# Optimization experiments

Measured on AMD Instinct MI355X. Metric: run time of the kernel, lower is better.

The kernel has to match this reference:

```python
import jax, jax.numpy as jnp
import numpy as np

B, C, L = 32, 64, 4096
LEVEL, FL, DIM, HID = 3, 8, 64, 64
MID = max(1, C // 4)
REG = 0.01
ODE_STEPS, ODE_H = 10, 0.1  # fixed-step integration of t in [0,1] (eval_t final point)


def _gelu(x):
    return jax.nn.gelu(x, approximate=False)  # torch nn.GELU default is exact erf


def _conv1d(x, w, b, pad, mode):
    # x: [B,Cin,L], w: [Cout,Cin,K] -> [B,Cout,L] (cross-correlation, like torch)
    if pad:
        x = jnp.pad(x, ((0, 0), (0, 0), (pad, pad)), mode=mode)
    y = jax.lax.conv_general_dilated(x, w, (1,), 'VALID',
                                     dimension_numbers=('NCH', 'OIH', 'NCH'))
    return y + b[None, :, None]


def _conv1x1(x, w, b):
    return jnp.einsum('oc,bcl->bol', w, x) + b[None, :, None]


def setup_inputs() -> dict:
    key = jax.random.key(0)
    ks = jax.random.split(key, 12)
    rn = lambda k, s: jax.random.normal(k, s, jnp.float32) * 0.05
    return {
        'x': jax.random.normal(ks[0], (B, C, L), jnp.float32),
        'ode_c1_w': rn(ks[1], (DIM, C, 3)),
        'ode_c1_b': jnp.zeros((DIM,), jnp.float32),
        'ode_c2_w': rn(ks[2], (C, DIM, 3)),
        'ode_c2_b': jnp.zeros((C,), jnp.float32),
        'damp': jnp.float32(0.01),
        'stat_w': rn(ks[3], (HID, C)),
        'stat_b': jnp.zeros((HID,), jnp.float32),
        'gen1_w': rn(ks[4], (2 * HID, HID)),
        'gen1_b': jnp.zeros((2 * HID,), jnp.float32),
        'gen2_w': rn(ks[5], (2 * FL, 2 * HID)),
        'gen2_b': jnp.zeros((2 * FL,), jnp.float32),
        'gate_w': rn(ks[6], (LEVEL, C, C, 3)),
        'gate_b': jnp.zeros((LEVEL, C), jnp.float32),
        'att_w1': rn(ks[7], (LEVEL - 1, MID, C)),
        'att_b1': jnp.zeros((LEVEL - 1, MID), jnp.float32),
        'att_w2': rn(ks[8], (LEVEL - 1, C, MID)),
        'att_b2': jnp.zeros((LEVEL - 1, C), jnp.float32),
    }


def _forward(x, ode_c1_w, ode_c1_b, ode_c2_w, ode_c2_b, damp,
             stat_w, stat_b, gen1_w, gen1_b, gen2_w, gen2_b,
             gate_w, gate_b, att_w1, att_b1, att_w2, att_b2):
    # --- WaveletODE_Pro: autonomous vector field, fixed-step RK4 over [0,1] ---
    def f(z):
        h = _gelu(_conv1d(z, ode_c1_w, ode_c1_b, 1, 'edge'))
        h = jnp.tanh(_conv1d(h, ode_c2_w, ode_c2_b, 1, 'edge'))
        return h - damp * z

    def rk4(z, _):
        k1 = f(z)
        k2 = f(z + 0.5 * ODE_H * k1)
        k3 = f(z + 0.5 * ODE_H * k2)
        k4 = f(z + ODE_H * k3)
        return z + (ODE_H / 6.0) * (k1 + 2 * k2 + 2 * k3 + k4), None

    x_evolved, _ = jax.lax.scan(rk4, x, None, length=ODE_STEPS)

    # --- DyWAN_Pro: per-sample wavelet filter generation + regularizers ---
    def dywan(a):
        stat = _gelu(a.mean(-1) @ stat_w.T + stat_b)               # [B,HID]
        g = _gelu(stat @ gen1_w.T + gen1_b) @ gen2_w.T + gen2_b     # [B,2F]
        lo, hi = g[:, :FL], g[:, FL:]
        lo_pad = jnp.pad(lo, ((0, 0), (1, 1)))                      # zero pad=1, kernel [-1,1]
        lo_smooth = jnp.abs(lo_pad[:, 1:] - lo_pad[:, :-1]).mean()
        lo_n = lo / (jnp.linalg.norm(lo, axis=1, keepdims=True) + 1e-8)
        shift = sum(jnp.abs(lo_n[:, :, None] * jnp.roll(lo_n, s, axis=1)[:, None, :]).mean()
                    for s in range(1, 4))
        amp = jnp.abs((lo_n ** 2).sum(1) - 1.0).mean()
        return lo, hi, REG * (shift + amp) + 0.1 * lo_smooth

    pad_l, pad_r = FL // 2, FL - FL // 2 - 1
    approx = x_evolved
    details, los, his = [], [], []
    ortho = jnp.float32(0.0)
    for _ in range(LEVEL):
        lo, hi, o = dywan(approx)
        ortho = ortho + o
        los.append(lo)
        his.append(hi)
        ap = jnp.pad(approx, ((0, 0), (0, 0), (pad_l, pad_r)), mode='edge')
        # per-sample filter shared across channels: grouped conv == windowed einsum
        win = jnp.stack([ap[:, :, k:k + L] for k in range(FL)], axis=-1)  # [B,C,L,F]
        new_approx = jnp.einsum('bclk,bk->bcl', win, lo)
        details.append(jnp.einsum('bclk,bk->bcl', win, hi))
        approx = new_approx

    # --- CrossScaleFusion: yl input is the INITIAL evolved approx (coeffs[0]) ---
    cur = x_evolved
    enhanced = []
    for i in range(LEVEL - 1, -1, -1):
        det = details[i]
        if i < LEVEL - 1:
            att = jax.nn.sigmoid(_conv1x1(_gelu(_conv1x1(cur, att_w1[i], att_b1[i])),
                                          att_w2[i], att_b2[i]))
            det = det * att + det
        gate = jax.nn.sigmoid(_conv1d(cur, gate_w[i], gate_b[i], 1, 'constant'))
        cur = cur + gate * det
        enhanced.append(det)
    enhanced.reverse()
    return (cur, enhanced[0], enhanced[1], enhanced[2], ortho,
            jnp.stack(los), jnp.stack(his))


def reference(x, ode_c1_w, ode_c1_b, ode_c2_w, ode_c2_b, damp,
              stat_w, stat_b, gen1_w, gen1_b, gen2_w, gen2_b,
              gate_w, gate_b, att_w1, att_b1, att_w2, att_b2):
    return _forward(x, ode_c1_w, ode_c1_b, ode_c2_w, ode_c2_b, damp,
                    stat_w, stat_b, gen1_w, gen1_b, gen2_w, gen2_b,
                    gate_w, gate_b, att_w1, att_b1, att_w2, att_b2)
```

## Files before the change

### kernel.cpp

```cpp
#include <hip/hip_runtime.h>

#define Bn   32
#define Cn   64
#define Ln   4096
#define Nn   (Bn*Cn*Ln)
#define FLn  8
#define MIDn 16
#define TILE3 64
#define NT   64

typedef __bf16 bf16_t;
typedef bf16_t bf16x4 __attribute__((ext_vector_type(4)));
typedef bf16_t bf16x8 __attribute__((ext_vector_type(8)));
typedef float  f32x4  __attribute__((ext_vector_type(4)));

__device__ __forceinline__ float tanh_fast(float x) {
    float t = __expf(2.0f * x);
    return 1.0f - __fdividef(2.0f, 1.0f + t);
}
__device__ __forceinline__ float gelu_fast(float x) {
    return __fdividef(x, 1.0f + __expf(-1.702f * x));
}
__device__ __forceinline__ float sigmoid_f(float x) {
    return 1.0f / (1.0f + __expf(-x));
}

__global__ __launch_bounds__(256) void prep_weights(
    const float* __restrict__ w1, const float* __restrict__ w2,
    const float* __restrict__ gw, const float* __restrict__ aw1,
    const float* __restrict__ aw2,
    bf16_t* __restrict__ w1f, bf16_t* __restrict__ w2f,
    bf16_t* __restrict__ gwf, bf16_t* __restrict__ aw1f,
    float* __restrict__ aw2t)
{
    int idx = blockIdx.x*256 + threadIdx.x;
    if (idx < 1536) {
        int lane = idx & 63;
        int f  = (idx >> 6) % 6;
        int mt = (idx >> 6) / 6;
        int tau = f >> 1, kc = f & 1;
        int oc = mt*16 + (lane & 15);
        int c0 = kc*32 + (lane >> 4)*8;
        #pragma unroll
        for (int e = 0; e < 8; ++e) {
            int c = c0 + e;
            w1f[idx*8 + e] = (bf16_t)w1[oc*192 + c*3 + tau];
            w2f[idx*8 + e] = (bf16_t)w2[oc*192 + c*3 + tau];
        }
    }
    if (idx < 4608) {
        int lane = idx & 63;
        int r  = idx >> 6;
        int f  = r % 6;
        int mt = (r / 6) % 4;
        int lvl = r / 24;
        int tau = f >> 1, kc = f & 1;
        int oc = mt*16 + (lane & 15);
        int c0 = kc*32 + (lane >> 4)*8;
        #pragma unroll
        for (int e = 0; e < 8; ++e)
            gwf[idx*8 + e] = (bf16_t)gw[((lvl*64 + oc)*64 + (c0+e))*3 + tau];
    }
    if (idx < 256) {
        int lane = idx & 63;
        int kc  = (idx >> 6) & 1;
        int lvl = idx >> 7;
        int mm = lane & 15;
        int c0 = kc*32 + (lane >> 4)*8;
        #pragma unroll
        for (int e = 0; e < 8; ++e)
            aw1f[idx*8 + e] = (bf16_t)aw1[lvl*1024 + mm*64 + c0 + e];
    }
    if (idx < 2*64*16) {
        int lvl = idx / 1024, rem = idx % 1024;
        int oc = rem / 16, mm = rem % 16;
        aw2t[lvl*1024 + mm*64 + oc] = aw2[idx];
    }
}

__global__ __launch_bounds__(256, 2) void ode_rk4_step(
    const float* __restrict__ zsrc, float* __restrict__ zdst,
    const bf16_t* __restrict__ w1f, const float* __restrict__ b1,
    const bf16_t* __restrict__ w2f, const float* __restrict__ b2,
    const float* __restrict__ damp_p)
{
    __shared__ bf16_t ZC[80*64];
    __shared__ bf16_t HT[80*64];
    __shared__ bf16_t Z0[80*64];
    __shared__ bf16_t SUMB[64*64];

    const int tid  = threadIdx.x;
    const int w    = tid >> 6;
    const int lane = tid & 63;
    const int c15  = lane & 15;
    const int hb   = lane >> 4;
    const int oc0  = w*16 + hb*4;
    const int b    = blockIdx.y;
    const int l0   = blockIdx.x * NT;
    const size_t bbase = (size_t)b * Cn * Ln;
    const float damp = damp_p[0];
    const int pmin = (blockIdx.x == 0) ? 8 : 0;
    const int pmax = (blockIdx.x == gridDim.x - 1) ? 71 : 79;

    #pragma unroll
    for (int jj = 0; jj < 4; ++jj) {
        const int cc0 = (w << 4) + jj*4;
        const float* zr0 = zsrc + bbase + (size_t)(cc0+0) * Ln;
        const float* zr1 = zsrc + bbase + (size_t)(cc0+1) * Ln;
        const float* zr2 = zsrc + bbase + (size_t)(cc0+2) * Ln;
        const float* zr3 = zsrc + bbase + (size_t)(cc0+3) * Ln;
        #pragma unroll
        for (int m2 = 0; m2 < 2; ++m2) {
            int p = lane + (m2 << 6);
            if (p < 80) {
                int l = l0 - 8 + p;
                l = l < 0 ? 0 : (l > Ln-1 ? Ln-1 : l);
                bf16x4 v;
                v[0] = (bf16_t)zr0[l]; v[1] = (bf16_t)zr1[l];
                v[2] = (bf16_t)zr2[l]; v[3] = (bf16_t)zr3[l];
                int off = p*64 + (cc0 ^ ((p & 7) << 3));
                *(bf16x4*)&ZC[off] = v;
                *(bf16x4*)&Z0[off] = v;
            }
        }
    }

    f32x4 bias1v, bias2v;
    #pragma unroll
    for (int j = 0; j < 4; ++j) {
        bias1v[j] = b1[oc0 + j];
        bias2v[j] = b2[oc0 + j];
    }
    bf16x8 af1[6], af2[6];
    {
        const bf16x8* wp1 = (const bf16x8*)w1f + (w*6)*64 + lane;
        const bf16x8* wp2 = (const bf16x8*)w2f + (w*6)*64 + lane;
        #pragma unroll
        for (int f = 0; f < 6; ++f) { af1[f] = wp1[f*64]; af2[f] = wp2[f*64]; }
    }

    __syncthreads();

    for (int i = 0; i < 4; ++i) {
        const int hLo = 2*i + 1, hHi = 79 - 2*i;
        const int kLo = 2*i + 2, kHi = 78 - 2*i;

        #pragma unroll
        for (int nt = 0; nt < 5; ++nt) {
            int ph = nt*16 + c15;
            f32x4 acc = bias1v;
            #pragma unroll
            for (int tau = 0; tau < 3; ++tau) {
                int p = ph + tau - 1;
                p = p < pmin ? pmin : (p > pmax ? pmax : p);
                int base = p*64 + ((hb*8) ^ ((p & 7) << 3));
                acc = __builtin_amdgcn_mfma_f32_16x16x32_bf16(
                    af1[tau*2+0], *(const bf16x8*)&ZC[base], acc, 0, 0, 0);
                acc = __builtin_amdgcn_mfma_f32_16x16x32_bf16(
                    af1[tau*2+1], *(const bf16x8*)&ZC[base ^ 32], acc, 0, 0, 0);
            }
            if (ph >= hLo && ph < hHi) {
                bf16x4 hv;
                #pragma unroll
                for (int j = 0; j < 4; ++j)
                    hv[j] = (bf16_t)gelu_fast(acc[j]);
                *(bf16x4*)&HT[ph*64 + (oc0 ^ ((ph & 7) << 3))] = hv;
            }
        }
        __syncthreads();

        #pragma unroll
        for (int nt = 0; nt < 5; ++nt) {
            int pk = nt*16 + c15;
            f32x4 acc = bias2v;
            #pragma unroll
            for (int tau = 0; tau < 3; ++tau) {
                int q = pk + tau - 1;
                q = q < pmin ? pmin : (q > pmax ? pmax : q);
                int base = q*64 + ((hb*8) ^ ((q & 7) << 3));
                acc = __builtin_amdgcn_mfma_f32_16x16x32_bf16(
                    af2[tau*2+0], *(const bf16x8*)&HT[base], acc, 0, 0, 0);
                acc = __builtin_amdgcn_mfma_f32_16x16x32_bf16(
                    af2[tau*2+1], *(const bf16x8*)&HT[base ^ 32], acc, 0, 0, 0);
            }
            const int col = oc0 ^ ((pk & 7) << 3);
            const int off = pk*64 + col;
            if (i < 3) {
                if (pk >= kLo && pk < kHi) {
                    bf16x4 zc = *(const bf16x4*)&ZC[off];
                    bf16x4 z0 = *(const bf16x4*)&Z0[off];
                    const float alpha = (i == 2) ? 0.10f : 0.05f;
                    const bool inS = (pk >= 8) && (pk < 72);
                    const int soff = (pk-8)*64 + col;
                    bf16x4 sv;
                    if (i > 0 && inS) sv = *(const bf16x4*)&SUMB[soff];
                    bf16x4 wv, nsv;
                    #pragma unroll
                    for (int j = 0; j < 4; ++j) {
                        float kv = tanh_fast(acc[j]) - damp * (float)zc[j];
                        wv[j]  = (bf16_t)((float)z0[j] + alpha * kv);
                        nsv[j] = (i == 0) ? (bf16_t)kv
                                          : (bf16_t)((float)sv[j] + 2.0f * kv);
                    }
                    *(bf16x4*)&ZC[off] = wv;
                    if (inS) *(bf16x4*)&SUMB[soff] = nsv;
                }
            } else {
                if (pk >= 8 && pk < 72) {
                    bf16x4 zc = *(const bf16x4*)&ZC[off];
                    bf16x4 sv = *(const bf16x4*)&SUMB[(pk-8)*64 + col];
                    int gcol = l0 + pk - 8;
                    #pragma unroll
                    for (int j = 0; j < 4; ++j) {
                        float kv = tanh_fast(acc[j]) - damp * (float)zc[j];
                        size_t gof = bbase + (size_t)(oc0 + j)*Ln + gcol;
                        zdst[gof] = zsrc[gof] + (0.1f/6.0f) * ((float)sv[j] + kv);
                    }
                }
            }
        }
        if (i < 3) __syncthreads();
    }
}

__global__ __launch_bounds__(256) void mean_kernel(const float* __restrict__ in, float* __restrict__ m)
{
    const int bc = blockIdx.x;
    const float* __restrict__ row = in + (size_t)bc*Ln;
    float s = 0.0f;
    for (int l = threadIdx.x; l < Ln; l += 256) s += row[l];
    #pragma unroll
    for (int off = 32; off > 0; off >>= 1) s += __shfl_down(s, off, 64);
    __shared__ float red[4];
    if ((threadIdx.x & 63) == 0) red[threadIdx.x >> 6] = s;
    __syncthreads();
    if (threadIdx.x == 0) m[bc] = red[0]+red[1]+red[2]+red[3];
}

__global__ __launch_bounds__(256) void dywan_kernel(
    const float* __restrict__ m,
    const float* __restrict__ stat_w, const float* __restrict__ stat_b,
    const float* __restrict__ gen1_w, const float* __restrict__ gen1_b,
    const float* __restrict__ gen2_w, const float* __restrict__ gen2_b,
    float* __restrict__ tail, int lvl)
{
    __shared__ float m_s[Bn][Cn];
    __shared__ float stat_s[Bn][64];
    __shared__ float g1_s[Bn][128];
    __shared__ float g_s[Bn][16];
    __shared__ float ored[Bn];
    const int tid = threadIdx.x;
    for (int i = tid; i < Bn*Cn; i += 256) m_s[i>>6][i&63] = m[i] * (1.0f/Ln);
    __syncthreads();
    for (int i = tid; i < Bn*64; i += 256) {
        int b = i >> 6, h = i & 63;
        float a = stat_b[h];
        for (int c = 0; c < Cn; ++c) a = fmaf(stat_w[h*64+c], m_s[b][c], a);
        stat_s[b][h] = 0.5f * a * (1.0f + erff(a * 0.7071067811865476f));
    }
    __syncthreads();
    for (int i = tid; i < Bn*128; i += 256) {
        int b = i >> 7, j = i & 127;
        float a = gen1_b[j];
        for (int h = 0; h < 64; ++h) a = fmaf(gen1_w[j*64+h], stat_s[b][h], a);
        g1_s[b][j] = 0.5f * a * (1.0f + erff(a * 0.7071067811865476f));
    }
    __syncthreads();
    for (int i = tid; i < Bn*16; i += 256) {
        int b = i >> 4, q = i & 15;
        float a = gen2_b[q];
        for (int j = 0; j < 128; ++j) a = fmaf(gen2_w[q*128+j], g1_s[b][j], a);
        g_s[b][q] = a;
    }
    __syncthreads();
    for (int i = tid; i < Bn*16; i += 256) {
        int b = i >> 4, q = i & 15;
        if (q < FLn) tail[1 + lvl*(Bn*FLn) + b*FLn + q] = g_s[b][q];
        else         tail[1 + 3*(Bn*FLn) + lvl*(Bn*FLn) + b*FLn + (q-FLn)] = g_s[b][q];
    }
    if (tid < Bn) {
        const int b = tid;
        float S1 = 0.f, n2 = 0.f, sm = 0.f, prev = 0.f;
        #pragma unroll
        for (int k = 0; k < FLn; ++k) {
            float v = g_s[b][k];
            S1 += fabsf(v); n2 = fmaf(v, v, n2);
            sm += fabsf(v - prev); prev = v;
        }
        sm += fabsf(prev);
        float den = sqrtf(n2) + 1e-8f;
        float Sn = S1 / den;
        float s2n = n2 / (den*den);
        ored[b] = 0.01f * (3.0f*Sn*Sn*(1.0f/2048.0f) + fabsf(s2n - 1.0f)*(1.0f/32.0f))
                + 0.1f * sm * (1.0f/288.0f);
    }
    __syncthreads();
    if (tid == 0) {
        float o = 0.f;
        for (int b = 0; b < Bn; ++b) o += ored[b];
        if (lvl == 0) tail[0] = o; else tail[0] += o;
    }
}

__global__ __launch_bounds__(256) void filter_kernel(
    const float* __restrict__ in, float* __restrict__ napprox,
    float* __restrict__ det,
    const float* __restrict__ lo, const float* __restrict__ hi,
    float* __restrict__ msum)
{
    const int bc = blockIdx.y;
    const int b = bc >> 6;
    float lov[8], hiv[8];
    #pragma unroll
    for (int k = 0; k < 8; ++k) { lov[k] = lo[b*8+k]; hiv[k] = hi[b*8+k]; }
    const float* __restrict__ row = in + (size_t)bc*Ln;
    const int l = blockIdx.x*256 + threadIdx.x;
    float na = 0.0f, dv = 0.0f;
    #pragma unroll
    for (int k = 0; k < 8; ++k) {
        int j = l + k - 4;
        j = j < 0 ? 0 : (j >= Ln ? Ln-1 : j);
        float v = row[j];
        na = fmaf(v, lov[k], na);
        dv = fmaf(v, hiv[k], dv);
    }
    size_t g = (size_t)bc*Ln + l;
    if (napprox) napprox[g] = na;
    det[g] = dv;
    if (msum) {
        float s = na;
        #pragma unroll
        for (int off = 32; off > 0; off >>= 1) s += __shfl_down(s, off, 64);
        __shared__ float red[4];
        if ((threadIdx.x & 63) == 0) red[threadIdx.x >> 6] = s;
        __syncthreads();
        if (threadIdx.x == 0)
            atomicAdd(&msum[bc], red[0]+red[1]+red[2]+red[3]);
    }
}

template<bool HAS_ATT>
__global__ __launch_bounds__(256, 2) void stage3_kernel(
    const float* __restrict__ cur_in, float* __restrict__ det,
    float* __restrict__ cur_out,
    const bf16_t* __restrict__ gwf, const float* __restrict__ gb,
    const bf16_t* __restrict__ aw1f, const float* __restrict__ ab1,
    const float* __restrict__ aw2t, const float* __restrict__ ab2)
{
    __shared__ bf16_t CB[66*64];
    __shared__ float t1_s[16][65];
    __shared__ float gate_s[64][65];
    __shared__ float att_s[64][65];

    const int tid  = threadIdx.x;
    const int w    = tid >> 6;
    const int lane = tid & 63;
    const int c15  = lane & 15;
    const int hb   = lane >> 4;
    const int oc0  = w*16 + hb*4;
    const int b    = blockIdx.y;
    const int l0   = blockIdx.x * TILE3;
    const size_t bbase = (size_t)b * Cn * Ln;

    #pragma unroll
    for (int jj = 0; jj < 4; ++jj) {
        const int cc0 = (w << 4) + jj*4;
        const float* cr0 = cur_in + bbase + (size_t)(cc0+0) * Ln;
        const float* cr1 = cur_in + bbase + (size_t)(cc0+1) * Ln;
        const float* cr2 = cur_in + bbase + (size_t)(cc0+2) * Ln;
        const float* cr3 = cur_in + bbase + (size_t)(cc0+3) * Ln;
        #pragma unroll
        for (int m2 = 0; m2 < 2; ++m2) {
            int p = lane + (m2 << 6);
            if (p < 66) {
                int l = l0 - 1 + p;
                bool in = (l >= 0) && (l < Ln);
                bf16x4 v;
                v[0] = (bf16_t)(in ? cr0[l] : 0.0f);
                v[1] = (bf16_t)(in ? cr1[l] : 0.0f);
                v[2] = (bf16_t)(in ? cr2[l] : 0.0f);
                v[3] = (bf16_t)(in ? cr3[l] : 0.0f);
                *(bf16x4*)&CB[p*64 + (cc0 ^ ((p & 7) << 3))] = v;
            }
        }
    }
    __syncthreads();

    if (HAS_ATT) {
        f32x4 acc;
        #pragma unroll
        for (int j = 0; j < 4; ++j) acc[j] = ab1[hb*4 + j];
        const int p = w*16 + c15 + 1;
        #pragma unroll
        for (int kc = 0; kc < 2; ++kc) {
            bf16x8 a1 = ((const bf16x8*)aw1f)[kc*64 + lane];
            int base = p*64 + (((kc*32) + hb*8) ^ ((p & 7) << 3));
            acc = __builtin_amdgcn_mfma_f32_16x16x32_bf16(
                a1, *(const bf16x8*)&CB[base], acc, 0, 0, 0);
        }
        #pragma unroll
        for (int j = 0; j < 4; ++j)
            t1_s[hb*4 + j][w*16 + c15] = gelu_fast(acc[j]);
    }

    {
        bf16x8 ag[6];
        const bf16x8* wp = (const bf16x8*)gwf + (w*6)*64 + lane;
        #pragma unroll
        for (int f = 0; f < 6; ++f) ag[f] = wp[f*64];
        f32x4 biasg;
        #pragma unroll
        for (int j = 0; j < 4; ++j) biasg[j] = gb[oc0 + j];

        #pragma unroll
        for (int nt = 0; nt < 5; ++nt) {
            int ph = nt*16 + c15;
            f32x4 acc = biasg;
            #pragma unroll
            for (int tau = 0; tau < 3; ++tau) {
                int q = ph - 1 + tau;
                q = q < 0 ? 0 : (q > 65 ? 65 : q);
                int base0 = q*64 + ((hb*8) ^ ((q & 7) << 3));
                acc = __builtin_amdgcn_mfma_f32_16x16x32_bf16(
                    ag[tau*2+0], *(const bf16x8*)&CB[base0], acc, 0, 0, 0);
                acc = __builtin_amdgcn_mfma_f32_16x16x32_bf16(
                    ag[tau*2+1], *(const bf16x8*)&CB[base0 ^ 32], acc, 0, 0, 0);
            }
            if (ph >= 1 && ph < 65) {
                int t = ph - 1;
                #pragma unroll
                for (int j = 0; j < 4; ++j)
                    gate_s[oc0 + j][t] = sigmoid_f(acc[j]);
            }
        }
    }
    __syncthreads();

    if (HAS_ATT) {
        const int oc = tid & 63;
        const int t0 = (tid >> 6) * 16;
        float w2r[16];
        #pragma unroll
        for (int mm = 0; mm < MIDn; ++mm) w2r[mm] = aw2t[mm*64 + oc];
        float av[16];
        const float bb = ab2[oc];
        #pragma unroll
        for (int j = 0; j < 16; ++j) av[j] = bb;
        #pragma unroll
        for (int mm = 0; mm < MIDn; ++mm) {
            #pragma unroll
            for (int j = 0; j < 16; ++j) av[j] = fmaf(w2r[mm], t1_s[mm][t0+j], av[j]);
        }
        #pragma unroll
        for (int j = 0; j < 16; ++j) att_s[oc][t0+j] = sigmoid_f(av[j]);
        __syncthreads();
    }

    const size_t gb0 = bbase + l0;
    for (int e = tid; e < Cn*TILE3; e += 256) {
        int c = e >> 6, t = e & 63;
        size_t g = gb0 + (size_t)c*Ln + t;
        float d = det[g];
        if (HAS_ATT) { d = d * (1.0f + att_s[c][t]); det[g] = d; }
        cur_out[g] = cur_in[g] + gate_s[c][t]*d;
    }
}

extern "C" void kernel_launch(void* const* d_in, const int* in_sizes, int n_in,
                              void* d_out, int out_size, void* d_ws, size_t ws_size,
                              hipStream_t stream)
{
    const float* x      = (const float*)d_in[0];
    const float* c1w    = (const float*)d_in[1];
    const float* c1b    = (const float*)d_in[2];
    const float* c2w    = (const float*)d_in[3];
    const float* c2b    = (const float*)d_in[4];
    const float* damp   = (const float*)d_in[5];
    const float* stat_w = (const float*)d_in[6];
    const float* stat_b = (const float*)d_in[7];
    const float* gen1_w = (const float*)d_in[8];
    const float* gen1_b = (const float*)d_in[9];
    const float* gen2_w = (const float*)d_in[10];
    const float* gen2_b = (const float*)d_in[11];
    const float* gate_w = (const float*)d_in[12];
    const float* gate_b = (const float*)d_in[13];
    const float* att_w1 = (const float*)d_in[14];
    const float* att_b1 = (const float*)d_in[15];
    const float* att_w2 = (const float*)d_in[16];
    const float* att_b2 = (const float*)d_in[17];

    float* out = (float*)d_out;
    float* Z    = (float*)d_ws;
    float* WSB  = Z + Nn;
    float* aw2t = WSB + Nn;
    float* m0   = aw2t + 2048;
    float* m1   = m0 + 2048;
    float* m2   = m1 + 2048;
    bf16_t* w1f  = (bf16_t*)(m2 + 2048);
    bf16_t* w2f  = w1f + 12288;
    bf16_t* gwf  = w2f + 12288;
    bf16_t* aw1f = gwf + 36864;

    float* tail = out + (size_t)4*Nn;

    prep_weights<<<144, 256, 0, stream>>>(c1w, c2w, gate_w, att_w1, att_w2,
                                          w1f, w2f, gwf, aw1f, aw2t);
    hipMemsetAsync(m1, 0, 2*2048*sizeof(float), stream);

    dim3 gOde(Ln/NT, Bn);
    for (int s = 0; s < 10; ++s) {
        const float* src = (s == 0) ? x : ((s & 1) ? Z : WSB);
        float*       dst = (s & 1) ? WSB : Z;
        ode_rk4_step<<<gOde, 256, 0, stream>>>(src, dst, w1f, c1b, w2f, c2b, damp);
    }

    dim3 gFil(Ln/256, Bn*Cn);
    const float* appr_in[3]  = {WSB, Z, out};
    float*       appr_out[3] = {Z, out, nullptr};
    float*       msum[3]     = {m1, m2, nullptr};
    float*       muse[3]     = {m0, m1, m2};
    mean_kernel<<<Bn*Cn, 256, 0, stream>>>(WSB, m0);
    for (int lvl = 0; lvl < 3; ++lvl) {
        dywan_kernel<<<1, 256, 0, stream>>>(muse[lvl], stat_w, stat_b, gen1_w, gen1_b,
                                            gen2_w, gen2_b, tail, lvl);
        filter_kernel<<<gFil, 256, 0, stream>>>(appr_in[lvl], appr_out[lvl],
            out + (size_t)(1+lvl)*Nn,
            tail + 1 + lvl*(Bn*FLn),
            tail + 1 + 3*(Bn*FLn) + lvl*(Bn*FLn),
            msum[lvl]);
    }

    dim3 gS3(Ln/TILE3, Bn);
    stage3_kernel<false><<<gS3, 256, 0, stream>>>(WSB, out + (size_t)3*Nn, Z,
        gwf + 2*12288, gate_b + 2*64, nullptr, nullptr, nullptr, nullptr);
    stage3_kernel<true><<<gS3, 256, 0, stream>>>(Z, out + (size_t)2*Nn, WSB,
        gwf + 1*12288, gate_b + 1*64, aw1f + 1024, att_b1 + 16, aw2t + 1024, att_b2 + 64);
    stage3_kernel<true><<<gS3, 256, 0, stream>>>(WSB, out + (size_t)1*Nn, out,
        gwf, gate_b, aw1f, att_b1, aw2t, att_b2);
}
```

Before: 1.186 ms.

## Fuse two RK4 steps per ODE kernel launch using wider halo tiles

The ODE kernel now performs two RK4 steps per launch, widening the shared-memory halo from 8 to 16 columns (96-wide tiles) so the intermediate state stays on chip. This halves the number of launches and the global round trips of the state tensor, and keeps the step-start state in fp32 in shared memory. In exchange, each block recomputes extra halo columns (6 instead of 5 column tiles per stage) and uses more LDS, which may lower occupancy.

```diff
diff --git a/kernel.cpp b/kernel.cpp
--- a/kernel.cpp
+++ b/kernel.cpp
@@ -7,7 +7,7 @@
 #define FLn  8
 #define MIDn 16
 #define TILE3 64
-#define NT   64
+#define NTD  64
 
 typedef __bf16 bf16_t;
 typedef bf16_t bf16x4 __attribute__((ext_vector_type(4)));
@@ -78,16 +78,16 @@
     }
 }
 
-__global__ __launch_bounds__(256, 2) void ode_rk4_step(
+__global__ __launch_bounds__(256, 2) void ode_rk4_2step(
     const float* __restrict__ zsrc, float* __restrict__ zdst,
     const bf16_t* __restrict__ w1f, const float* __restrict__ b1,
     const bf16_t* __restrict__ w2f, const float* __restrict__ b2,
     const float* __restrict__ damp_p)
 {
-    __shared__ bf16_t ZC[80*64];
-    __shared__ bf16_t HT[80*64];
-    __shared__ bf16_t Z0[80*64];
-    __shared__ bf16_t SUMB[64*64];
+    __shared__ bf16_t ZC[96*64];
+    __shared__ bf16_t HT[96*64];
+    __shared__ float  Z0F[96*64];
+    __shared__ bf16_t SUMB[80*64];
 
     const int tid  = threadIdx.x;
     const int w    = tid >> 6;
@@ -96,11 +96,11 @@
     const int hb   = lane >> 4;
     const int oc0  = w*16 + hb*4;
     const int b    = blockIdx.y;
-    const int l0   = blockIdx.x * NT;
+    const int l0   = blockIdx.x * NTD;
     const size_t bbase = (size_t)b * Cn * Ln;
     const float damp = damp_p[0];
-    const int pmin = (blockIdx.x == 0) ? 8 : 0;
-    const int pmax = (blockIdx.x == gridDim.x - 1) ? 71 : 79;
+    const int pmin = (blockIdx.x == 0) ? 16 : 0;
+    const int pmax = (blockIdx.x == gridDim.x - 1) ? 79 : 95;
 
     #pragma unroll
     for (int jj = 0; jj < 4; ++jj) {
@@ -112,15 +112,18 @@
         #pragma unroll
         for (int m2 = 0; m2 < 2; ++m2) {
             int p = lane + (m2 << 6);
-            if (p < 80) {
-                int l = l0 - 8 + p;
+            if (p < 96) {
+                int l = l0 - 16 + p;
                 l = l < 0 ? 0 : (l > Ln-1 ? Ln-1 : l);
-                bf16x4 v;
-                v[0] = (bf16_t)zr0[l]; v[1] = (bf16_t)zr1[l];
-                v[2] = (bf16_t)zr2[l]; v[3] = (bf16_t)zr3[l];
+                f32x4 vf;
+                vf[0] = zr0[l]; vf[1] = zr1[l];
+                vf[2] = zr2[l]; vf[3] = zr3[l];
                 int off = p*64 + (cc0 ^ ((p & 7) << 3));
-                *(bf16x4*)&ZC[off] = v;
-                *(bf16x4*)&Z0[off] = v;
+                bf16x4 vb;
+                #pragma unroll
+                for (int e = 0; e < 4; ++e) vb[e] = (bf16_t)vf[e];
+                *(bf16x4*)&ZC[off] = vb;
+                *(f32x4*)&Z0F[off] = vf;
             }
         }
     }
@@ -141,12 +144,13 @@
 
     __syncthreads();
 
-    for (int i = 0; i < 4; ++i) {
-        const int hLo = 2*i + 1, hHi = 79 - 2*i;
-        const int kLo = 2*i + 2, kHi = 78 - 2*i;
-
-        #pragma unroll
-        for (int nt = 0; nt < 5; ++nt) {
+    for (int i = 0; i < 8; ++i) {
+        const int hLo = 2*i + 1, hHi = 95 - 2*i;
+        const int kLo = 2*i + 2, kHi = 94 - 2*i;
+        const int ii  = i & 3;
+
+        #pragma unroll
+        for (int nt = 0; nt < 6; ++nt) {
             int ph = nt*16 + c15;
             f32x4 acc = bias1v;
             #pragma unroll
@@ -170,7 +174,7 @@
         __syncthreads();
 
         #pragma unroll
-        for (int nt = 0; nt < 5; ++nt) {
+        for (int nt = 0; nt < 6; ++nt) {
             int pk = nt*16 + c15;
             f32x4 acc = bias2v;
             #pragma unroll
@@ -183,43 +187,51 @@
                 acc = __builtin_amdgcn_mfma_f32_16x16x32_bf16(
                     af2[tau*2+1], *(const bf16x8*)&HT[base ^ 32], acc, 0, 0, 0);
             }
-            const int col = oc0 ^ ((pk & 7) << 3);
-            const int off = pk*64 + col;
-            if (i < 3) {
-                if (pk >= kLo && pk < kHi) {
-                    bf16x4 zc = *(const bf16x4*)&ZC[off];
-                    bf16x4 z0 = *(const bf16x4*)&Z0[off];
-                    const float alpha = (i == 2) ? 0.10f : 0.05f;
-                    const bool inS = (pk >= 8) && (pk < 72);
-                    const int soff = (pk-8)*64 + col;
+            if (pk >= kLo && pk < kHi) {
+                const int col = oc0 ^ ((pk & 7) << 3);
+                const int off = pk*64 + col;
+                const int soff = (pk-8)*64 + col;
+                bf16x4 zc = *(const bf16x4*)&ZC[off];
+                f32x4  z0 = *(const f32x4*)&Z0F[off];
+                if (ii < 3) {
+                    const float alpha = (ii == 2) ? 0.10f : 0.05f;
                     bf16x4 sv;
-                    if (i > 0 && inS) sv = *(const bf16x4*)&SUMB[soff];
+                    if (ii > 0) sv = *(const bf16x4*)&SUMB[soff];
                     bf16x4 wv, nsv;
                     #pragma unroll
                     for (int j = 0; j < 4; ++j) {
                         float kv = tanh_fast(acc[j]) - damp * (float)zc[j];
-                        wv[j]  = (bf16_t)((float)z0[j] + alpha * kv);
-                        nsv[j] = (i == 0) ? (bf16_t)kv
-                                          : (bf16_t)((float)sv[j] + 2.0f * kv);
+                        wv[j]  = (bf16_t)(z0[j] + alpha * kv);
+                        nsv[j] = (ii == 0) ? (bf16_t)kv
+                                           : (bf16_t)((float)sv[j] + 2.0f * kv);
                     }
                     *(bf16x4*)&ZC[off] = wv;
-                    if (inS) *(bf16x4*)&SUMB[soff] = nsv;
-                }
-            } else {
-                if (pk >= 8 && pk < 72) {
-                    bf16x4 zc = *(const bf16x4*)&ZC[off];
-                    bf16x4 sv = *(const bf16x4*)&SUMB[(pk-8)*64 + col];
-                    int gcol = l0 + pk - 8;
-                    #pragma unroll
-                    for (int j = 0; j < 4; ++j) {
-                        float kv = tanh_fast(acc[j]) - damp * (float)zc[j];
-                        size_t gof = bbase + (size_t)(oc0 + j)*Ln + gcol;
-                        zdst[gof] = zsrc[gof] + (0.1f/6.0f) * ((float)sv[j] + kv);
+                    *(bf16x4*)&SUMB[soff] = nsv;
+                } else {
+                    bf16x4 sv = *(const bf16x4*)&SUMB[soff];
+                    if (i == 3) {
+                        f32x4 z1; bf16x4 zb;
+                        #pragma unroll
+                        for (int j = 0; j < 4; ++j) {
+                            float kv = tanh_fast(acc[j]) - damp * (float)zc[j];
+                            z1[j] = z0[j] + (0.1f/6.0f) * ((float)sv[j] + kv);
+                            zb[j] = (bf16_t)z1[j];
+                        }
+                        *(f32x4*)&Z0F[off] = z1;
+                        *(bf16x4*)&ZC[off] = zb;
+                    } else {
+                        int gcol = l0 + pk - 16;
+                        #pragma unroll
+                        for (int j = 0; j < 4; ++j) {
+                            float kv = tanh_fast(acc[j]) - damp * (float)zc[j];
+                            size_t gof = bbase + (size_t)(oc0 + j)*Ln + gcol;
+                            zdst[gof] = z0[j] + (0.1f/6.0f) * ((float)sv[j] + kv);
+                        }
                     }
                 }
             }
         }
-        if (i < 3) __syncthreads();
+        if (i < 7) __syncthreads();
     }
 }
 
@@ -507,12 +519,12 @@
                                           w1f, w2f, gwf, aw1f, aw2t);
     hipMemsetAsync(m1, 0, 2*2048*sizeof(float), stream);
 
-    dim3 gOde(Ln/NT, Bn);
-    for (int s = 0; s < 10; ++s) {
-        const float* src = (s == 0) ? x : ((s & 1) ? Z : WSB);
-        float*       dst = (s & 1) ? WSB : Z;
-        ode_rk4_step<<<gOde, 256, 0, stream>>>(src, dst, w1f, c1b, w2f, c2b, damp);
-    }
+    dim3 gOde(Ln/NTD, Bn);
+    ode_rk4_2step<<<gOde, 256, 0, stream>>>(x,   WSB, w1f, c1b, w2f, c2b, damp);
+    ode_rk4_2step<<<gOde, 256, 0, stream>>>(WSB, Z,   w1f, c1b, w2f, c2b, damp);
+    ode_rk4_2step<<<gOde, 256, 0, stream>>>(Z,   WSB, w1f, c1b, w2f, c2b, damp);
+    ode_rk4_2step<<<gOde, 256, 0, stream>>>(WSB, Z,   w1f, c1b, w2f, c2b, damp);
+    ode_rk4_2step<<<gOde, 256, 0, stream>>>(Z,   WSB, w1f, c1b, w2f, c2b, damp);
 
     dim3 gFil(Ln/256, Bn*Cn);
     const float* appr_in[3]  = {WSB, Z, out};
```

Measured after the change: 1.157 ms. -2.5%, faster.
